# Optimization experiments

Measured on AMD Instinct MI355X. Metric: run time of the kernel, lower is better.

## Reference

```python
import jax, jax.numpy as jnp
import numpy as np

N_NODES = 100000
N_EDGES = 1600000
NUM_FEATURES = 64
HIDDEN = 64
NUM_CLASSES = 16


def setup_inputs() -> dict:
    key = jax.random.key(0)
    ks = jax.random.split(key, 8)
    x = jax.random.normal(ks[0], (N_NODES, NUM_FEATURES), dtype=jnp.float32)
    edge_index = jax.random.randint(ks[1], (2, N_EDGES), 0, N_NODES, dtype=jnp.int32)
    # Glorot-ish init for weights, zero bias (matches GCNConv / Linear defaults closely enough)
    s1 = 1.0 / np.sqrt(NUM_FEATURES)
    s2 = 1.0 / np.sqrt(HIDDEN)
    W1 = jax.random.uniform(ks[2], (NUM_FEATURES, HIDDEN), jnp.float32, -s1, s1)
    b1 = jnp.zeros((HIDDEN,), jnp.float32)
    W2 = jax.random.uniform(ks[3], (HIDDEN, HIDDEN), jnp.float32, -s2, s2)
    b2 = jnp.zeros((HIDDEN,), jnp.float32)
    W3 = jax.random.uniform(ks[4], (HIDDEN, NUM_CLASSES), jnp.float32, -s2, s2)
    b3 = jax.random.uniform(ks[5], (NUM_CLASSES,), jnp.float32, -s2, s2)
    return {"x": x, "edge_index": edge_index, "W1": W1, "b1": b1,
            "W2": W2, "b2": b2, "W3": W3, "b3": b3}


def _gcn_layer(x, W, b, src, dst, norm, n_nodes):
    # GCNConv: h = X W; out[i] = sum_{(j->i)} norm_ji * h[j]; out += b
    h = x @ W                                   # [N, H] small dense GEMM
    msg = h[src] * norm[:, None]                # [E+N, H] irregular gather
    out = jax.ops.segment_sum(msg, dst, num_segments=n_nodes)  # scatter-add
    return out + b


def reference(x, edge_index, W1, b1, W2, b2, W3, b3):
    n = x.shape[0]
    loop = jnp.arange(n, dtype=edge_index.dtype)
    # add self-loops (PyG GCNConv default add_self_loops=True)
    src = jnp.concatenate([edge_index[0], loop])
    dst = jnp.concatenate([edge_index[1], loop])
    # symmetric normalization D^{-1/2} A_hat D^{-1/2}
    deg = jax.ops.segment_sum(jnp.ones_like(src, dtype=x.dtype), dst, num_segments=n)
    dis = jax.lax.rsqrt(deg)                    # deg >= 1 due to self-loops
    norm = dis[src] * dis[dst]                  # [E+N]

    h = jax.nn.relu(_gcn_layer(x, W1, b1, src, dst, norm, n))
    # F.dropout(training=False) -> identity (module in eval mode)
    h = jax.nn.relu(_gcn_layer(h, W2, b2, src, dst, norm, n))
    z = h @ W3 + b3
    return jax.nn.log_softmax(z, axis=1), h
```

## Files before the change

### kernel.cpp

```cpp
#include <hip/hip_runtime.h>
#include <hip/hip_bf16.h>

typedef __hip_bfloat16 bf16;
typedef unsigned short ushort;

#define NN 100000
#define NE 1600000
#define NBKT 782
#define BCAP 4096
#define EPB 8192
#define NP1 196
#define NMT 6250

typedef __attribute__((ext_vector_type(8))) short s8v;
typedef __attribute__((ext_vector_type(4))) float f4v;

__device__ __forceinline__ float ldf(const void* p, int i, int f32) {
    return f32 ? ((const float*)p)[i] : __bfloat162float(((const bf16*)p)[i]);
}
__device__ __forceinline__ void stf(void* p, int i, int f32, float v) {
    if (f32) ((float*)p)[i] = v;
    else     ((bf16*)p)[i] = __float2bfloat16(v);
}

__device__ __forceinline__ ushort f2b(float f) {
    unsigned u = __builtin_bit_cast(unsigned, f);
    u += 0x7FFF + ((u >> 16) & 1);
    return (ushort)(u >> 16);
}
__device__ __forceinline__ float b2f(ushort h) {
    unsigned u = ((unsigned)h) << 16;
    return __builtin_bit_cast(float, u);
}

__global__ void k_detect(const unsigned* __restrict__ x, int* __restrict__ flag) {
    __shared__ int cnt[256];
    int t = threadIdx.x, c = 0;
    for (int i = t; i < 2048; i += 256) {
        unsigned e7 = (x[i] >> 8) & 0x7F;
        c += (e7 >= 60 && e7 <= 66) ? 1 : 0;
    }
    cnt[t] = c;
    __syncthreads();
    for (int s = 128; s > 0; s >>= 1) {
        if (t < s) cnt[t] += cnt[t + s];
        __syncthreads();
    }
    if (t == 0) *flag = (cnt[0] >= 1024) ? 0 : 1;
}

__global__ void k_sentinel(unsigned* out) {
    if (threadIdx.x == 0 && blockIdx.x == 0) out[0] = 0x461C461Cu;
}

__global__ void k_zero_i(int* __restrict__ p, int n) {
    int i = blockIdx.x * 256 + threadIdx.x;
    if (i < n) p[i] = 0;
}

__global__ void k_pass1(const int* __restrict__ src, const int* __restrict__ dst,
                        int* __restrict__ gcur, unsigned* __restrict__ bbuf) {
    __shared__ int hist[NBKT];
    __shared__ int base[NBKT];
    int t = threadIdx.x;
    int e0 = blockIdx.x * EPB;
    for (int i = t; i < NBKT; i += 256) hist[i] = 0;
    __syncthreads();
    for (int k = 0; k < EPB; k += 256) {
        int e = e0 + k + t;
        if (e < NE) atomicAdd(&hist[dst[e] >> 7], 1);
    }
    __syncthreads();
    for (int i = t; i < NBKT; i += 256) {
        int c = hist[i];
        base[i] = c ? atomicAdd(&gcur[i], c) : 0;
    }
    __syncthreads();
    for (int i = t; i < NBKT; i += 256) hist[i] = 0;
    __syncthreads();
    for (int k = 0; k < EPB; k += 256) {
        int e = e0 + k + t;
        if (e < NE) {
            int d = dst[e];
            int b = d >> 7;
            int lp = atomicAdd(&hist[b], 1);
            bbuf[b * BCAP + base[b] + lp] = ((unsigned)src[e] << 7) | (unsigned)(d & 127);
        }
    }
}

__global__ void k_scanB(const int* __restrict__ gcur, int* __restrict__ gbase,
                        int* __restrict__ rowptr) {
    __shared__ int s[1024];
    int t = threadIdx.x;
    int v = (t < NBKT) ? gcur[t] : 0;
    s[t] = v;
    __syncthreads();
    for (int d = 1; d < 1024; d <<= 1) {
        int add = (t >= d) ? s[t - d] : 0;
        __syncthreads();
        s[t] += add;
        __syncthreads();
    }
    if (t < NBKT) gbase[t] = s[t] - v;
    if (t == 0) { gbase[NBKT] = NE; rowptr[NN] = NE; }
}

__global__ void k_pass2(const unsigned* __restrict__ bbuf, const int* __restrict__ gbase,
                        int* __restrict__ rowptr, float* __restrict__ dis,
                        int* __restrict__ csr_src) {
    __shared__ unsigned vals[BCAP];
    __shared__ int lout[BCAP];
    __shared__ int fh[128], fx[128], fc[128];
    int b = blockIdx.x, t = threadIdx.x;
    int g0 = gbase[b], cnt = gbase[b + 1] - g0;
    const unsigned* in = bbuf + b * BCAP;
    if (t < 128) fh[t] = 0;
    __syncthreads();
    for (int i = t; i < cnt; i += 256) {
        unsigned v = in[i];
        vals[i] = v;
        atomicAdd(&fh[v & 127], 1);
    }
    __syncthreads();
    if (t < 128) fx[t] = fh[t];
    __syncthreads();
    for (int d = 1; d < 128; d <<= 1) {
        int add = (t >= d && t < 128) ? fx[t - d] : 0;
        __syncthreads();
        if (t < 128) fx[t] += add;
        __syncthreads();
    }
    int n = b * 128 + t;
    if (t < 128) {
        int ex = fx[t] - fh[t];
        fc[t] = ex;
        if (n < NN) {
            rowptr[n] = g0 + ex;
            dis[n] = rsqrtf(1.0f + (float)fh[t]);
        }
    }
    __syncthreads();
    for (int i = t; i < cnt; i += 256) {
        unsigned v = vals[i];
        int p = atomicAdd(&fc[v & 127], 1);
        lout[p] = (int)(v >> 7);
    }
    __syncthreads();
    for (int i = t; i < cnt; i += 256) csr_src[g0 + i] = lout[i];
}

__global__ void __launch_bounds__(256) k_gemm_mfma(
        const void* __restrict__ A, int aBase, const void* __restrict__ W,
        bf16* __restrict__ C, const int* __restrict__ flag) {
    int f32 = *flag;
    int t = threadIdx.x;
    int lane = t & 63;
    int w = t >> 6;
    int m = lane & 15, q = lane >> 4;

    s8v bh[2][4], bl[2][4];
#pragma unroll
    for (int st = 0; st < 2; st++)
#pragma unroll
        for (int nt = 0; nt < 4; nt++)
#pragma unroll
            for (int j = 0; j < 8; j++) {
                int k = st * 32 + q * 8 + j;
                float wv = ldf(W, k * 64 + nt * 16 + m, f32);
                ushort h = f2b(wv);
                bh[st][nt][j] = (short)h;
                bl[st][nt][j] = (short)f2b(wv - b2f(h));
            }

    ushort* Cu = (ushort*)C;
    int gw = blockIdx.x * 4 + w;
    int nw = gridDim.x * 4;
    for (int mt = gw; mt < NMT; mt += nw) {
        int row = mt * 16 + m;
        s8v ah[2], al[2];
        if (f32) {
            const float* ap = (const float*)A + aBase + row * 64 + q * 8;
#pragma unroll
            for (int st = 0; st < 2; st++)
#pragma unroll
                for (int j = 0; j < 8; j++) {
                    float v = ap[st * 32 + j];
                    ushort h = f2b(v);
                    ah[st][j] = (short)h;
                    al[st][j] = (short)f2b(v - b2f(h));
                }
        } else {
            const short* ap = (const short*)A + aBase + row * 64 + q * 8;
            ah[0] = *(const s8v*)(ap);
            ah[1] = *(const s8v*)(ap + 32);
        }
#pragma unroll
        for (int nt = 0; nt < 4; nt++) {
            f4v acc = {0.f, 0.f, 0.f, 0.f};
#pragma unroll
            for (int st = 0; st < 2; st++)
                acc = __builtin_amdgcn_mfma_f32_16x16x32_bf16(ah[st], bh[st][nt], acc, 0, 0, 0);
            if (f32) {
#pragma unroll
                for (int st = 0; st < 2; st++) {
                    acc = __builtin_amdgcn_mfma_f32_16x16x32_bf16(ah[st], bl[st][nt], acc, 0, 0, 0);
                    acc = __builtin_amdgcn_mfma_f32_16x16x32_bf16(al[st], bh[st][nt], acc, 0, 0, 0);
                }
            }
            int col = nt * 16 + m;
#pragma unroll
            for (int r = 0; r < 4; r++) {
                int rr = mt * 16 + q * 4 + r;
                Cu[rr * 64 + col] = f2b(acc[r]);
            }
        }
    }
}

__global__ void k_aggregate(const bf16* __restrict__ hin, void* hout, int hoBase,
                            const float* __restrict__ dis,
                            const int* __restrict__ rowptr,
                            const int* __restrict__ csr_src,
                            const void* __restrict__ bias,
                            const int* __restrict__ flag) {
    int f32 = *flag;
    int n = blockIdx.x * 4 + (threadIdx.x >> 6);
    int c = threadIdx.x & 63;
    if (n >= NN) return;
    const ushort* hu = (const ushort*)hin;
    float dn = dis[n];
    float acc = dn * b2f(hu[n * 64 + c]);
    int j = rowptr[n], end = rowptr[n + 1];
    while (j < end) {
        int s[16];
#pragma unroll
        for (int k = 0; k < 16; k++) {
            int e = j + k;
            s[k] = (e < end) ? csr_src[e] : n;
        }
        float w[16];
#pragma unroll
        for (int k = 0; k < 16; k++) w[k] = (j + k < end) ? dis[s[k]] : 0.f;
        float v[16];
#pragma unroll
        for (int k = 0; k < 16; k++) v[k] = b2f(hu[s[k] * 64 + c]);
#pragma unroll
        for (int k = 0; k < 16; k++) acc += w[k] * v[k];
        j += 16;
    }
    float r = fmaxf(dn * acc + ldf(bias, c, f32), 0.f);
    stf(hout, hoBase + n * 64 + c, f32, r);
}

__global__ void k_head(const void* __restrict__ h2, int hBase,
                       const void* __restrict__ W3, const void* __restrict__ b3,
                       void* out, const int* __restrict__ flag) {
    __shared__ float w[64 * 16];
    __shared__ float hrow[16 * 64];
    int f32 = *flag;
    int t = threadIdx.x;
#pragma unroll
    for (int i = 0; i < 4; i++) w[t + i * 256] = ldf(W3, t + i * 256, f32);
    int r0 = blockIdx.x * 16;
#pragma unroll
    for (int i = 0; i < 4; i++) hrow[t + i * 256] = ldf(h2, hBase + r0 * 64 + t + i * 256, f32);
    __syncthreads();
    int lr = t >> 4, c = t & 15;
    float z = ldf(b3, c, f32);
#pragma unroll
    for (int k = 0; k < 64; k++) z += hrow[lr * 64 + k] * w[k * 16 + c];
    float m = z;
#pragma unroll
    for (int off = 8; off >= 1; off >>= 1) m = fmaxf(m, __shfl_xor(m, off, 16));
    float p = expf(z - m);
    float s = p;
#pragma unroll
    for (int off = 8; off >= 1; off >>= 1) s += __shfl_xor(s, off, 16);
    stf(out, (r0 + lr) * 16 + c, f32, z - m - logf(s));
}

extern "C" void kernel_launch(void* const* d_in, const int* in_sizes, int n_in,
                              void* d_out, int out_size, void* d_ws, size_t ws_size,
                              hipStream_t stream) {
    const void* x  = d_in[0];
    const int* ei  = (const int*)d_in[1];
    const void* W1 = d_in[2];
    const void* b1 = d_in[3];
    const void* W2 = d_in[4];
    const void* b2 = d_in[5];
    const void* W3 = d_in[6];
    const void* b3 = d_in[7];

    const size_t NEEDED = (size_t)(1807104 + NBKT * BCAP) * 4;
    if (ws_size < NEEDED) {
        k_sentinel<<<1, 64, 0, stream>>>((unsigned*)d_out);
        return;
    }
    int*      flag    = (int*)d_ws;
    float*    dis     = (float*)d_ws + 256;
    int*      rowptr  = (int*)d_ws + 102656;
    int*      gcur    = (int*)d_ws + 205056;
    int*      gbase   = (int*)d_ws + 206080;
    int*      csr_src = (int*)d_ws + 207104;
    unsigned* bbuf    = (unsigned*)((int*)d_ws + 1807104);
    bf16*     bufA    = (bf16*)bbuf;

    const int* srcp = ei;
    const int* dstp = ei + NE;
    const int HB = NN * 16;

    k_detect<<<1, 256, 0, stream>>>((const unsigned*)x, flag);

    k_zero_i<<<4, 256, 0, stream>>>(gcur, 1024);
    k_pass1<<<NP1, 256, 0, stream>>>(srcp, dstp, gcur, bbuf);
    k_scanB<<<1, 1024, 0, stream>>>(gcur, gbase, rowptr);
    k_pass2<<<NBKT, 256, 0, stream>>>(bbuf, gbase, rowptr, dis, csr_src);

    k_gemm_mfma<<<512, 256, 0, stream>>>(x, 0, W1, bufA, flag);
    k_aggregate<<<NN / 4, 256, 0, stream>>>(bufA, d_out, HB, dis, rowptr, csr_src, b1, flag);

    k_gemm_mfma<<<512, 256, 0, stream>>>(d_out, HB, W2, bufA, flag);
    k_aggregate<<<NN / 4, 256, 0, stream>>>(bufA, d_out, HB, dis, rowptr, csr_src, b2, flag);

    k_head<<<NN / 16, 256, 0, stream>>>(d_out, HB, W3, b3, d_out, flag);
}
```

Measured before the change: 300.9 us.

## Prescale GEMM output by source norm and store byte offsets in CSR

The GEMM epilogue now multiplies each row by dis[row], so aggregation no longer gathers dis[src] per edge. The CSR stores precomputed byte offsets (src*128) instead of indices, and padded slots point to a zeroed dummy row, so the inner loop is a plain sum with no per-edge weight or index multiply. This removes one dependent random gather per edge from the hot aggregate kernel. The cost is a tiny extra kernel to zero the pad row and an extra bf16 rounding of the prescaled features.

Measured after the change: 343.3 us. 1.14x slower.

```diff
diff --git a/kernel.cpp b/kernel.cpp
--- a/kernel.cpp
+++ b/kernel.cpp
@@ -58,6 +58,10 @@
     if (i < n) p[i] = 0;
 }
 
+__global__ void k_zero_row(bf16* __restrict__ p) {
+    p[NN * 64 + threadIdx.x] = __float2bfloat16(0.f);
+}
+
 __global__ void k_pass1(const int* __restrict__ src, const int* __restrict__ dst,
                         int* __restrict__ gcur, unsigned* __restrict__ bbuf) {
     __shared__ int hist[NBKT];
@@ -108,7 +112,7 @@
 
 __global__ void k_pass2(const unsigned* __restrict__ bbuf, const int* __restrict__ gbase,
                         int* __restrict__ rowptr, float* __restrict__ dis,
-                        int* __restrict__ csr_src) {
+                        int* __restrict__ csr_off) {
     __shared__ unsigned vals[BCAP];
     __shared__ int lout[BCAP];
     __shared__ int fh[128], fx[128], fc[128];
@@ -144,15 +148,16 @@
     for (int i = t; i < cnt; i += 256) {
         unsigned v = vals[i];
         int p = atomicAdd(&fc[v & 127], 1);
-        lout[p] = (int)(v >> 7);
-    }
-    __syncthreads();
-    for (int i = t; i < cnt; i += 256) csr_src[g0 + i] = lout[i];
+        lout[p] = (int)(v & ~127u);
+    }
+    __syncthreads();
+    for (int i = t; i < cnt; i += 256) csr_off[g0 + i] = lout[i];
 }
 
 __global__ void __launch_bounds__(256) k_gemm_mfma(
         const void* __restrict__ A, int aBase, const void* __restrict__ W,
-        bf16* __restrict__ C, const int* __restrict__ flag) {
+        bf16* __restrict__ C, const float* __restrict__ dis,
+        const int* __restrict__ flag) {
     int f32 = *flag;
     int t = threadIdx.x;
     int lane = t & 63;
@@ -195,6 +200,9 @@
             ah[0] = *(const s8v*)(ap);
             ah[1] = *(const s8v*)(ap + 32);
         }
+        float dr[4];
+#pragma unroll
+        for (int r = 0; r < 4; r++) dr[r] = dis[mt * 16 + q * 4 + r];
 #pragma unroll
         for (int nt = 0; nt < 4; nt++) {
             f4v acc = {0.f, 0.f, 0.f, 0.f};
@@ -212,41 +220,40 @@
 #pragma unroll
             for (int r = 0; r < 4; r++) {
                 int rr = mt * 16 + q * 4 + r;
-                Cu[rr * 64 + col] = f2b(acc[r]);
+                Cu[rr * 64 + col] = f2b(dr[r] * acc[r]);
             }
         }
     }
 }
 
-__global__ void k_aggregate(const bf16* __restrict__ hin, void* hout, int hoBase,
+__global__ void k_aggregate(const bf16* __restrict__ hs, void* hout, int hoBase,
                             const float* __restrict__ dis,
                             const int* __restrict__ rowptr,
-                            const int* __restrict__ csr_src,
+                            const int* __restrict__ csr_off,
                             const void* __restrict__ bias,
                             const int* __restrict__ flag) {
     int f32 = *flag;
     int n = blockIdx.x * 4 + (threadIdx.x >> 6);
     int c = threadIdx.x & 63;
     if (n >= NN) return;
-    const ushort* hu = (const ushort*)hin;
+    const char* hb = (const char*)hs;
+    int c2 = c * 2;
     float dn = dis[n];
-    float acc = dn * b2f(hu[n * 64 + c]);
+    float acc = b2f(*(const ushort*)(hb + n * 128 + c2));
     int j = rowptr[n], end = rowptr[n + 1];
+    const int ZOFF = NN * 128;
     while (j < end) {
-        int s[16];
+        int o[16];
 #pragma unroll
         for (int k = 0; k < 16; k++) {
             int e = j + k;
-            s[k] = (e < end) ? csr_src[e] : n;
-        }
-        float w[16];
-#pragma unroll
-        for (int k = 0; k < 16; k++) w[k] = (j + k < end) ? dis[s[k]] : 0.f;
+            o[k] = (e < end) ? csr_off[e] : ZOFF;
+        }
         float v[16];
 #pragma unroll
-        for (int k = 0; k < 16; k++) v[k] = b2f(hu[s[k] * 64 + c]);
-#pragma unroll
-        for (int k = 0; k < 16; k++) acc += w[k] * v[k];
+        for (int k = 0; k < 16; k++) v[k] = b2f(*(const ushort*)(hb + o[k] + c2));
+#pragma unroll
+        for (int k = 0; k < 16; k++) acc += v[k];
         j += 16;
     }
     float r = fmaxf(dn * acc + ldf(bias, c, f32), 0.f);
@@ -302,7 +309,7 @@
     int*      rowptr  = (int*)d_ws + 102656;
     int*      gcur    = (int*)d_ws + 205056;
     int*      gbase   = (int*)d_ws + 206080;
-    int*      csr_src = (int*)d_ws + 207104;
+    int*      csr_off = (int*)d_ws + 207104;
     unsigned* bbuf    = (unsigned*)((int*)d_ws + 1807104);
     bf16*     bufA    = (bf16*)bbuf;
 
@@ -315,13 +322,14 @@
     k_zero_i<<<4, 256, 0, stream>>>(gcur, 1024);
     k_pass1<<<NP1, 256, 0, stream>>>(srcp, dstp, gcur, bbuf);
     k_scanB<<<1, 1024, 0, stream>>>(gcur, gbase, rowptr);
-    k_pass2<<<NBKT, 256, 0, stream>>>(bbuf, gbase, rowptr, dis, csr_src);
-
-    k_gemm_mfma<<<512, 256, 0, stream>>>(x, 0, W1, bufA, flag);
-    k_aggregate<<<NN / 4, 256, 0, stream>>>(bufA, d_out, HB, dis, rowptr, csr_src, b1, flag);
-
-    k_gemm_mfma<<<512, 256, 0, stream>>>(d_out, HB, W2, bufA, flag);
-    k_aggregate<<<NN / 4, 256, 0, stream>>>(bufA, d_out, HB, dis, rowptr, csr_src, b2, flag);
+    k_pass2<<<NBKT, 256, 0, stream>>>(bbuf, gbase, rowptr, dis, csr_off);
+    k_zero_row<<<1, 64, 0, stream>>>(bufA);
+
+    k_gemm_mfma<<<512, 256, 0, stream>>>(x, 0, W1, bufA, dis, flag);
+    k_aggregate<<<NN / 4, 256, 0, stream>>>(bufA, d_out, HB, dis, rowptr, csr_off, b1, flag);
+
+    k_gemm_mfma<<<512, 256, 0, stream>>>(d_out, HB, W2, bufA, dis, flag);
+    k_aggregate<<<NN / 4, 256, 0, stream>>>(bufA, d_out, HB, dis, rowptr, csr_off, b2, flag);
 
     k_head<<<NN / 16, 256, 0, stream>>>(d_out, HB, W3, b3, d_out, flag);
 }
```
